# Kernel optimization log

Measured on AMD Instinct MI355X. Metric: run time of the kernel, lower is better.

Reference implementation:

```python
import jax, jax.numpy as jnp
import numpy as np

B = 32
NODES = [200000, 1024, 256, 32]
CH = [1, 32, 64, 128]
EDGES = [2048000, 262144, 8192]
NCLS = 10


def _wn(V, g):
    # PyTorch weight_norm (dim=0): each output row rescaled to norm g[o]
    return g[:, None] * V / jnp.linalg.norm(V, axis=1, keepdims=True)


def _fgl(x, src, dst, n_out, W, b):
    # x: (B, C_in, N_in); sparse random-adjacency downsample then channel mix
    xt = jnp.moveaxis(x, 2, 0)                                   # (N_in, B, C_in)
    gathered = xt[src]                                           # (E, B, C_in)
    pooled = jax.ops.segment_sum(gathered, dst, num_segments=n_out)  # (N_out, B, C_in)
    return jnp.einsum('nbc,oc->bon', pooled, W) + b[None, :, None]   # (B, C_out, N_out)


def setup_inputs() -> dict:
    key = jax.random.key(0)
    ks = jax.random.split(key, 20)
    d = {}
    d['x'] = jax.random.normal(ks[0], (B, NODES[0]), jnp.float32)
    for i in range(3):
        e = EDGES[i]
        n_in, n_out = NODES[i], NODES[i + 1]
        d[f'edge_src{i}'] = jax.random.randint(ks[1 + 2 * i], (e,), 0, n_in, jnp.int32)
        d[f'edge_dst{i}'] = jnp.sort(jax.random.randint(ks[2 + 2 * i], (e,), 0, n_out, jnp.int32))
    for i in range(3):
        cin, cout = CH[i], CH[i + 1]
        d[f'V{i}'] = jax.random.normal(ks[7 + 3 * i], (cout, cin), jnp.float32) * 0.1
        d[f'g{i}'] = jnp.ones((cout,), jnp.float32)
        d[f'b{i}'] = jnp.zeros((cout,), jnp.float32)
    d['Vfc'] = jax.random.normal(ks[16], (NCLS, CH[-1] * NODES[-1]), jnp.float32) * 0.02
    d['gfc'] = jnp.ones((NCLS,), jnp.float32)
    d['bfc'] = jnp.zeros((NCLS,), jnp.float32)
    return d


def reference(x, edge_src0, edge_dst0, edge_src1, edge_dst1, edge_src2, edge_dst2,
              V0, g0, b0, V1, g1, b1, V2, g2, b2, Vfc, gfc, bfc):
    z = x[:, None, :]                                            # (B, 1, N_in)
    z = _fgl(z, edge_src0, edge_dst0, NODES[1], _wn(V0, g0), b0)  # (B, 32, 1024)
    z = _fgl(z, edge_src1, edge_dst1, NODES[2], _wn(V1, g1), b1)  # (B, 64, 256)
    z = _fgl(z, edge_src2, edge_dst2, NODES[3], _wn(V2, g2), b2)  # (B, 128, 32)
    flat = z.reshape(z.shape[0], -1)                             # (B, 4096)
    return flat @ _wn(Vfc, gfc).T + bfc                          # (B, NCLS)
```

## Files before the change

kernel.cpp:

```cpp
#include <hip/hip_runtime.h>
#include <math.h>

#define N0 200000
#define N1 1024
#define N2 256
#define N3 32
#define NE0 2048000
#define NE1 262144
#define NE2 8192
#define BATCH 32
#define NCLS 10
#define NB 4
#define SRC_PER_B 50000

typedef _Float16 h2 __attribute__((ext_vector_type(2)));
typedef _Float16 h8 __attribute__((ext_vector_type(8)));

__device__ __forceinline__ int lower_bound_i(const int* __restrict__ a, int n, int key) {
    int lo = 0, hi = n;
    while (lo < hi) {
        int mid = (lo + hi) >> 1;
        if (a[mid] < key) lo = mid + 1; else hi = mid;
    }
    return lo;
}

__global__ __launch_bounds__(256) void k_transpose(const float* __restrict__ x,
                                                   h2* __restrict__ xt) {
    __shared__ float tile[32][65];
    const int col0 = blockIdx.x * 64;
    const int tid = threadIdx.x;
    const int c = tid & 63, r0 = tid >> 6;
    #pragma unroll
    for (int r = r0; r < 32; r += 4) {
        int col = col0 + c;
        tile[r][c] = (col < N0) ? x[r * N0 + col] : 0.f;
    }
    __syncthreads();
    const int bb = (tid & 15) * 2, c0 = tid >> 4;
    #pragma unroll
    for (int cc = c0; cc < 64; cc += 16) {
        int col = col0 + cc;
        if (col < N0) {
            h2 v;
            v[0] = (_Float16)tile[bb][cc];
            v[1] = (_Float16)tile[bb + 1][cc];
            xt[col * 16 + (bb >> 1)] = v;
        }
    }
}

__global__ __launch_bounds__(256) void k_bounds(const int* __restrict__ dst,
                                                int* __restrict__ off) {
    int e = blockIdx.x * 256 + threadIdx.x;
    if (e >= NE0) return;
    int d = dst[e];
    int dp = (e == 0) ? -1 : dst[e - 1];
    for (int n = dp + 1; n <= d; ++n) off[n] = e;
    if (e == NE0 - 1) {
        for (int n = d + 1; n <= N1; ++n) off[n] = NE0;
    }
}

__global__ __launch_bounds__(256) void k_partition(const int* __restrict__ src,
                                                   const int* __restrict__ off,
                                                   int* __restrict__ esrc,
                                                   int* __restrict__ bstart) {
    const int n = blockIdx.x;
    const int e0 = off[n];
    const int e1 = off[n + 1];
    const int len = e1 - e0;
    const int tid = threadIdx.x;
    const int wave = tid >> 6, lane = tid & 63;
    const int q0 = e0 + (len * wave) / 4;
    const int q1 = e0 + (len * (wave + 1)) / 4;
    __shared__ int wcnt[4][NB];
    __shared__ int wbase[4][NB];

    int c0 = 0, c1 = 0, c2 = 0, c3 = 0;
    for (int base = q0; base < q1; base += 64) {
        int e = base + lane;
        int b = -1;
        if (e < q1) b = src[e] / SRC_PER_B;
        c0 += __popcll(__ballot(b == 0));
        c1 += __popcll(__ballot(b == 1));
        c2 += __popcll(__ballot(b == 2));
        c3 += __popcll(__ballot(b == 3));
    }
    if (lane == 0) { wcnt[wave][0] = c0; wcnt[wave][1] = c1; wcnt[wave][2] = c2; wcnt[wave][3] = c3; }
    __syncthreads();
    if (tid == 0) {
        int acc = e0;
        #pragma unroll
        for (int b = 0; b < NB; ++b) {
            bstart[n * (NB + 1) + b] = acc;
            #pragma unroll
            for (int w = 0; w < 4; ++w) { wbase[w][b] = acc; acc += wcnt[w][b]; }
        }
        bstart[n * (NB + 1) + NB] = acc;
    }
    __syncthreads();

    int u0 = wbase[wave][0], u1 = wbase[wave][1], u2 = wbase[wave][2], u3 = wbase[wave][3];
    for (int base = q0; base < q1; base += 64) {
        int e = base + lane;
        int s = 0, b = -1;
        if (e < q1) { s = src[e]; b = s / SRC_PER_B; }
        unsigned long long m0 = __ballot(b == 0);
        unsigned long long m1 = __ballot(b == 1);
        unsigned long long m2 = __ballot(b == 2);
        unsigned long long m3 = __ballot(b == 3);
        unsigned long long lt = (1ull << lane) - 1ull;
        if (b == 0)      esrc[u0 + __popcll(m0 & lt)] = s;
        else if (b == 1) esrc[u1 + __popcll(m1 & lt)] = s;
        else if (b == 2) esrc[u2 + __popcll(m2 & lt)] = s;
        else if (b == 3) esrc[u3 + __popcll(m3 & lt)] = s;
        u0 += __popcll(m0); u1 += __popcll(m1); u2 += __popcll(m2); u3 += __popcll(m3);
    }
}

__global__ __launch_bounds__(64) void k_gather0s(const h8* __restrict__ table,
                                                 const int* __restrict__ esrc,
                                                 const int* __restrict__ bstart,
                                                 float* __restrict__ part) {
    const int b = blockIdx.x & (NB - 1);
    const int n = blockIdx.x >> 2;
    const int q0 = bstart[n * (NB + 1) + b];
    const int q1 = bstart[n * (NB + 1) + b + 1];
    const int lane = threadIdx.x;
    const int b4 = lane & 3;
    const int g  = lane >> 2;
    float acc[8] = {0.f, 0.f, 0.f, 0.f, 0.f, 0.f, 0.f, 0.f};
    int e = q0 + g;
    for (; e + 48 < q1; e += 64) {
        int s0 = __builtin_nontemporal_load(esrc + e);
        int s1 = __builtin_nontemporal_load(esrc + e + 16);
        int s2 = __builtin_nontemporal_load(esrc + e + 32);
        int s3 = __builtin_nontemporal_load(esrc + e + 48);
        h8 v0 = table[s0 * 4 + b4];
        h8 v1 = table[s1 * 4 + b4];
        h8 v2 = table[s2 * 4 + b4];
        h8 v3 = table[s3 * 4 + b4];
        #pragma unroll
        for (int i = 0; i < 8; ++i)
            acc[i] += (float)v0[i] + (float)v1[i] + (float)v2[i] + (float)v3[i];
    }
    for (; e < q1; e += 16) {
        int s = __builtin_nontemporal_load(esrc + e);
        h8 v = table[s * 4 + b4];
        #pragma unroll
        for (int i = 0; i < 8; ++i) acc[i] += (float)v[i];
    }
    #pragma unroll
    for (int off = 4; off <= 32; off <<= 1) {
        #pragma unroll
        for (int i = 0; i < 8; ++i) acc[i] += __shfl_xor(acc[i], off);
    }
    if (g == 0) {
        float4 lo = make_float4(acc[0], acc[1], acc[2], acc[3]);
        float4 hi = make_float4(acc[4], acc[5], acc[6], acc[7]);
        float4* p4 = reinterpret_cast<float4*>(part + (size_t)(b * N1 + n) * 32 + b4 * 8);
        p4[0] = lo; p4[1] = hi;
    }
}

__global__ __launch_bounds__(256) void k_reduceP(const float* __restrict__ part,
                                                 _Float16* __restrict__ out) {
    int i = blockIdx.x * 256 + threadIdx.x;
    float s = part[i] + part[N1 * 32 + i] + part[2 * N1 * 32 + i] + part[3 * N1 * 32 + i];
    out[i] = (_Float16)s;
}

__global__ __launch_bounds__(256) void k_gather(const h8* __restrict__ table,
                                                const int* __restrict__ src,
                                                const int* __restrict__ dst,
                                                int nedges,
                                                _Float16* __restrict__ out_h,
                                                float* __restrict__ out_f,
                                                const float* __restrict__ cnt_in,
                                                float* __restrict__ cnt_out,
                                                float* __restrict__ t_out) {
    const int n = blockIdx.x;
    const int e0 = lower_bound_i(dst, nedges, n);
    const int e1 = lower_bound_i(dst, nedges, n + 1);
    const int tid = threadIdx.x;
    const int b4 = tid & 3;
    const int g  = tid >> 2;
    float acc[8] = {0.f, 0.f, 0.f, 0.f, 0.f, 0.f, 0.f, 0.f};
    float tacc = 0.f;
    int e = e0 + g;
    for (; e + 192 < e1; e += 256) {
        int s0 = __builtin_nontemporal_load(src + e);
        int s1 = __builtin_nontemporal_load(src + e + 64);
        int s2 = __builtin_nontemporal_load(src + e + 128);
        int s3 = __builtin_nontemporal_load(src + e + 192);
        h8 v0 = table[s0 * 4 + b4];
        h8 v1 = table[s1 * 4 + b4];
        h8 v2 = table[s2 * 4 + b4];
        h8 v3 = table[s3 * 4 + b4];
        #pragma unroll
        for (int i = 0; i < 8; ++i)
            acc[i] += (float)v0[i] + (float)v1[i] + (float)v2[i] + (float)v3[i];
        if (cnt_in != nullptr && b4 == 0)
            tacc += cnt_in[s0] + cnt_in[s1] + cnt_in[s2] + cnt_in[s3];
    }
    for (; e < e1; e += 64) {
        int s = __builtin_nontemporal_load(src + e);
        h8 v = table[s * 4 + b4];
        #pragma unroll
        for (int i = 0; i < 8; ++i) acc[i] += (float)v[i];
        if (cnt_in != nullptr && b4 == 0) tacc += cnt_in[s];
    }
    __shared__ float red[64][33];
    __shared__ float tred[64];
    #pragma unroll
    for (int i = 0; i < 8; ++i) red[g][b4 * 8 + i] = acc[i];
    if (b4 == 0) tred[g] = tacc;
    __syncthreads();
    #pragma unroll
    for (int s = 32; s >= 1; s >>= 1) {
        if (g < s) {
            #pragma unroll
            for (int i = 0; i < 8; ++i)
                red[g][b4 * 8 + i] += red[g + s][b4 * 8 + i];
            if (b4 == 0) tred[g] += tred[g + s];
        }
        __syncthreads();
    }
    if (tid < 32) {
        float v = red[0][tid];
        if (out_h != nullptr) out_h[n * 32 + tid] = (_Float16)v;
        if (out_f != nullptr) out_f[n * 32 + tid] = v;
    } else if (tid == 32 && cnt_out != nullptr) {
        cnt_out[n] = (float)(e1 - e0);
    } else if (tid == 33 && t_out != nullptr) {
        t_out[n] = tred[0];
    }
}

__global__ __launch_bounds__(256) void k_out(
    const float* __restrict__ V0, const float* __restrict__ g0, const float* __restrict__ b0,
    const float* __restrict__ V1, const float* __restrict__ g1, const float* __restrict__ b1,
    const float* __restrict__ V2, const float* __restrict__ g2, const float* __restrict__ b2,
    const float* __restrict__ Vfc, const float* __restrict__ gfc, const float* __restrict__ bfc,
    const float* __restrict__ S2, const float* __restrict__ T2, const float* __restrict__ cnt2,
    float* __restrict__ out) {
    const int k = blockIdx.x;
    const int tid = threadIdx.x;
    __shared__ float w0[32], u[64], v[64], p[128], q[128], r[128];
    __shared__ float redA[8][32], redB[8][32], redC[8][32], redD[8][32];
    __shared__ float nnred[4];
    __shared__ float M[32];
    __shared__ float scale_s, Kc_s;

    if (tid < 32) {
        float val = V0[tid];
        w0[tid] = g0[tid] * val / fabsf(val);
    }
    __syncthreads();
    if (tid < 64) {
        float nn = 0.f;
        #pragma unroll
        for (int c = 0; c < 32; ++c) { float t = V1[tid * 32 + c]; nn += t * t; }
        float inv = g1[tid] * rsqrtf(nn);
        float su = 0.f, sv = 0.f;
        #pragma unroll
        for (int c = 0; c < 32; ++c) {
            float w = V1[tid * 32 + c] * inv;
            su += w * w0[c]; sv += w * b0[c];
        }
        u[tid] = su; v[tid] = sv;
    }
    __syncthreads();
    if (tid < 128) {
        float nn = 0.f;
        #pragma unroll
        for (int c = 0; c < 64; ++c) { float t = V2[tid * 64 + c]; nn += t * t; }
        float inv = g2[tid] * rsqrtf(nn);
        float sp = 0.f, sq = 0.f, sr = 0.f;
        #pragma unroll
        for (int c = 0; c < 64; ++c) {
            float w = V2[tid * 64 + c] * inv;
            sp += w * u[c]; sq += w * v[c]; sr += w * b1[c];
        }
        p[tid] = sp; q[tid] = sq; r[tid] = sr;
    }
    __syncthreads();

    const int n3 = tid & 31, og = tid >> 5;
    float nn = 0.f, mk = 0.f, mq = 0.f, mr = 0.f, mb = 0.f;
    #pragma unroll
    for (int i = 0; i < 16; ++i) {
        int o = og + 8 * i;
        float w = Vfc[k * 4096 + tid + 256 * i];
        nn += w * w;
        mk += w * p[o]; mq += w * q[o]; mr += w * r[o]; mb += w * b2[o];
    }
    #pragma unroll
    for (int off = 32; off; off >>= 1) nn += __shfl_xor(nn, off);
    if ((tid & 63) == 0) nnred[tid >> 6] = nn;
    redA[og][n3] = mk; redB[og][n3] = mq; redC[og][n3] = mr; redD[og][n3] = mb;
    __syncthreads();
    if (tid == 0) {
        float s = nnred[0] + nnred[1] + nnred[2] + nnred[3];
        scale_s = gfc[k] * rsqrtf(s);
    }
    __syncthreads();
    if (tid < 32) {
        float smk = 0.f, smq = 0.f, smr = 0.f, smb = 0.f;
        #pragma unroll
        for (int i = 0; i < 8; ++i) {
            smk += redA[i][tid]; smq += redB[i][tid];
            smr += redC[i][tid]; smb += redD[i][tid];
        }
        float scale = scale_s;
        M[tid] = scale * smk;
        float kcp = scale * (smq * T2[tid] + smr * cnt2[tid] + smb);
        #pragma unroll
        for (int off = 16; off; off >>= 1) kcp += __shfl_xor(kcp, off);
        if (tid == 0) Kc_s = kcp + bfc[k];
    }
    __syncthreads();
    if (tid < 32) {
        int b = tid;
        float s = 0.f;
        #pragma unroll
        for (int n = 0; n < 32; ++n) s += M[n] * S2[n * 32 + b];
        out[b * NCLS + k] = s + Kc_s;
    }
}

extern "C" void kernel_launch(void* const* d_in, const int* in_sizes, int n_in,
                              void* d_out, int out_size, void* d_ws, size_t ws_size,
                              hipStream_t stream) {
    const float* x   = (const float*)d_in[0];
    const int* src0  = (const int*)d_in[1];
    const int* dst0  = (const int*)d_in[2];
    const int* src1  = (const int*)d_in[3];
    const int* dst1  = (const int*)d_in[4];
    const int* src2  = (const int*)d_in[5];
    const int* dst2  = (const int*)d_in[6];
    const float* V0  = (const float*)d_in[7];
    const float* g0  = (const float*)d_in[8];
    const float* b0  = (const float*)d_in[9];
    const float* V1  = (const float*)d_in[10];
    const float* g1  = (const float*)d_in[11];
    const float* b1  = (const float*)d_in[12];
    const float* V2  = (const float*)d_in[13];
    const float* g2  = (const float*)d_in[14];
    const float* b2  = (const float*)d_in[15];
    const float* Vfc = (const float*)d_in[16];
    const float* gfc = (const float*)d_in[17];
    const float* bfc = (const float*)d_in[18];

    char* ws = (char*)d_ws;
    _Float16* xt  = (_Float16*)(ws);
    int* esrc     = (int*)(ws + 12800000);
    int* off      = (int*)(ws + 20992000);
    int* bstart   = (int*)(ws + 20996352);
    float* P0p    = (float*)(ws + 21016832);
    _Float16* P0h = (_Float16*)(ws + 21541120);
    _Float16* S1h = (_Float16*)(ws + 21606656);
    float* cnt1   = (float*)(ws + 21623040);
    float* S2     = (float*)(ws + 21624064);
    float* T2     = (float*)(ws + 21628160);
    float* cnt2   = (float*)(ws + 21628288);

    k_transpose<<<(N0 + 63) / 64, 256, 0, stream>>>(x, (h2*)xt);
    k_bounds<<<NE0 / 256, 256, 0, stream>>>(dst0, off);
    k_partition<<<N1, 256, 0, stream>>>(src0, off, esrc, bstart);
    k_gather0s<<<N1 * NB, 64, 0, stream>>>((const h8*)xt, esrc, bstart, P0p);
    k_reduceP<<<(N1 * 32) / 256, 256, 0, stream>>>(P0p, P0h);
    k_gather<<<N2, 256, 0, stream>>>((const h8*)P0h, src1, dst1, NE1,
                                     S1h, nullptr, nullptr, cnt1, nullptr);
    k_gather<<<N3, 256, 0, stream>>>((const h8*)S1h, src2, dst2, NE2,
                                     nullptr, S2, cnt1, cnt2, T2);
    k_out<<<NCLS, 256, 0, stream>>>(V0, g0, b0, V1, g1, b1, V2, g2, b2,
                                    Vfc, gfc, bfc, S2, T2, cnt2, (float*)d_out);
}
```

Before: 77.78 us.

## Fuse small tail kernels, drop bounds pass, last-block reduction in gather0

Removes the k_bounds pass by having k_partition binary-search dst0 directly, and folds k_reduceP into k_gather0s through an atomic last-block-done counter. The layer-2 gather and the output projection are merged into one 1024-thread k_tail kernel. k_gather0s also moves to 128-thread blocks with a shared-memory reduction. The aim is to cut kernel launch count and tiny-grid launch overhead, at the cost of serialising the final reduction on one block and running the tail on a single CU.

```diff
diff --git a/kernel.cpp b/kernel.cpp
--- a/kernel.cpp
+++ b/kernel.cpp
@@ -12,6 +12,7 @@
 #define NCLS 10
 #define NB 4
 #define SRC_PER_B 50000
+#define G0_BLOCKS (N1 * NB)
 
 typedef _Float16 h2 __attribute__((ext_vector_type(2)));
 typedef _Float16 h8 __attribute__((ext_vector_type(8)));
@@ -50,27 +51,17 @@
     }
 }
 
-__global__ __launch_bounds__(256) void k_bounds(const int* __restrict__ dst,
-                                                int* __restrict__ off) {
-    int e = blockIdx.x * 256 + threadIdx.x;
-    if (e >= NE0) return;
-    int d = dst[e];
-    int dp = (e == 0) ? -1 : dst[e - 1];
-    for (int n = dp + 1; n <= d; ++n) off[n] = e;
-    if (e == NE0 - 1) {
-        for (int n = d + 1; n <= N1; ++n) off[n] = NE0;
-    }
-}
-
 __global__ __launch_bounds__(256) void k_partition(const int* __restrict__ src,
-                                                   const int* __restrict__ off,
+                                                   const int* __restrict__ dst,
                                                    int* __restrict__ esrc,
-                                                   int* __restrict__ bstart) {
+                                                   int* __restrict__ bstart,
+                                                   int* __restrict__ gcnt) {
     const int n = blockIdx.x;
-    const int e0 = off[n];
-    const int e1 = off[n + 1];
+    const int tid = threadIdx.x;
+    if (n == 0 && tid == 0) *gcnt = 0;
+    const int e0 = lower_bound_i(dst, NE0, n);
+    const int e1 = lower_bound_i(dst, NE0, n + 1);
     const int len = e1 - e0;
-    const int tid = threadIdx.x;
     const int wave = tid >> 6, lane = tid & 63;
     const int q0 = e0 + (len * wave) / 4;
     const int q1 = e0 + (len * (wave + 1)) / 4;
@@ -119,24 +110,26 @@
     }
 }
 
-__global__ __launch_bounds__(64) void k_gather0s(const h8* __restrict__ table,
-                                                 const int* __restrict__ esrc,
-                                                 const int* __restrict__ bstart,
-                                                 float* __restrict__ part) {
+__global__ __launch_bounds__(128) void k_gather0s(const h8* __restrict__ table,
+                                                  const int* __restrict__ esrc,
+                                                  const int* __restrict__ bstart,
+                                                  float* __restrict__ part,
+                                                  _Float16* __restrict__ p0h,
+                                                  int* __restrict__ gcnt) {
     const int b = blockIdx.x & (NB - 1);
     const int n = blockIdx.x >> 2;
     const int q0 = bstart[n * (NB + 1) + b];
     const int q1 = bstart[n * (NB + 1) + b + 1];
-    const int lane = threadIdx.x;
-    const int b4 = lane & 3;
-    const int g  = lane >> 2;
+    const int tid = threadIdx.x;
+    const int b4 = tid & 3;
+    const int g  = tid >> 2;
     float acc[8] = {0.f, 0.f, 0.f, 0.f, 0.f, 0.f, 0.f, 0.f};
     int e = q0 + g;
-    for (; e + 48 < q1; e += 64) {
+    for (; e + 96 < q1; e += 128) {
         int s0 = __builtin_nontemporal_load(esrc + e);
-        int s1 = __builtin_nontemporal_load(esrc + e + 16);
-        int s2 = __builtin_nontemporal_load(esrc + e + 32);
-        int s3 = __builtin_nontemporal_load(esrc + e + 48);
+        int s1 = __builtin_nontemporal_load(esrc + e + 32);
+        int s2 = __builtin_nontemporal_load(esrc + e + 64);
+        int s3 = __builtin_nontemporal_load(esrc + e + 96);
         h8 v0 = table[s0 * 4 + b4];
         h8 v1 = table[s1 * 4 + b4];
         h8 v2 = table[s2 * 4 + b4];
@@ -145,55 +138,71 @@
         for (int i = 0; i < 8; ++i)
             acc[i] += (float)v0[i] + (float)v1[i] + (float)v2[i] + (float)v3[i];
     }
-    for (; e < q1; e += 16) {
+    for (; e < q1; e += 32) {
         int s = __builtin_nontemporal_load(esrc + e);
         h8 v = table[s * 4 + b4];
         #pragma unroll
         for (int i = 0; i < 8; ++i) acc[i] += (float)v[i];
     }
-    #pragma unroll
-    for (int off = 4; off <= 32; off <<= 1) {
-        #pragma unroll
-        for (int i = 0; i < 8; ++i) acc[i] += __shfl_xor(acc[i], off);
-    }
-    if (g == 0) {
-        float4 lo = make_float4(acc[0], acc[1], acc[2], acc[3]);
-        float4 hi = make_float4(acc[4], acc[5], acc[6], acc[7]);
-        float4* p4 = reinterpret_cast<float4*>(part + (size_t)(b * N1 + n) * 32 + b4 * 8);
-        p4[0] = lo; p4[1] = hi;
-    }
-}
-
-__global__ __launch_bounds__(256) void k_reduceP(const float* __restrict__ part,
-                                                 _Float16* __restrict__ out) {
-    int i = blockIdx.x * 256 + threadIdx.x;
-    float s = part[i] + part[N1 * 32 + i] + part[2 * N1 * 32 + i] + part[3 * N1 * 32 + i];
-    out[i] = (_Float16)s;
-}
-
-__global__ __launch_bounds__(256) void k_gather(const h8* __restrict__ table,
-                                                const int* __restrict__ src,
-                                                const int* __restrict__ dst,
-                                                int nedges,
-                                                _Float16* __restrict__ out_h,
-                                                float* __restrict__ out_f,
-                                                const float* __restrict__ cnt_in,
-                                                float* __restrict__ cnt_out,
-                                                float* __restrict__ t_out) {
+    __shared__ float red[32][33];
+    #pragma unroll
+    for (int i = 0; i < 8; ++i) red[g][b4 * 8 + i] = acc[i];
+    __syncthreads();
+    #pragma unroll
+    for (int s = 16; s >= 1; s >>= 1) {
+        if (g < s) {
+            #pragma unroll
+            for (int i = 0; i < 8; ++i)
+                red[g][b4 * 8 + i] += red[g + s][b4 * 8 + i];
+        }
+        __syncthreads();
+    }
+    if (tid < 32) part[(b * N1 + n) * 32 + tid] = red[0][tid];
+
+    __shared__ int isLast;
+    __threadfence();
+    __syncthreads();
+    if (tid == 0) {
+        int old = atomicAdd(gcnt, 1);
+        isLast = (old == G0_BLOCKS - 1) ? 1 : 0;
+    }
+    __syncthreads();
+    if (isLast) {
+        __threadfence();
+        const float4* p4 = (const float4*)part;
+        h2* out2 = (h2*)p0h;
+        for (int i = tid; i < 8192; i += 128) {
+            float4 a = p4[i], c = p4[8192 + i], d = p4[16384 + i], f = p4[24576 + i];
+            float sx = a.x + c.x + d.x + f.x;
+            float sy = a.y + c.y + d.y + f.y;
+            float sz = a.z + c.z + d.z + f.z;
+            float sw = a.w + c.w + d.w + f.w;
+            h2 lo; lo[0] = (_Float16)sx; lo[1] = (_Float16)sy;
+            h2 hi; hi[0] = (_Float16)sz; hi[1] = (_Float16)sw;
+            out2[i * 2] = lo; out2[i * 2 + 1] = hi;
+        }
+        if (tid == 0) *gcnt = 0;
+    }
+}
+
+__global__ __launch_bounds__(256) void k_gather1(const h8* __restrict__ table,
+                                                 const int* __restrict__ src,
+                                                 const int* __restrict__ dst,
+                                                 _Float16* __restrict__ out_h,
+                                                 float* __restrict__ cnt_out) {
     const int n = blockIdx.x;
-    const int e0 = lower_bound_i(dst, nedges, n);
-    const int e1 = lower_bound_i(dst, nedges, n + 1);
+    const int e0 = lower_bound_i(dst, NE1, n);
+    const int e1 = lower_bound_i(dst, NE1, n + 1);
     const int tid = threadIdx.x;
     const int b4 = tid & 3;
     const int g  = tid >> 2;
     float acc[8] = {0.f, 0.f, 0.f, 0.f, 0.f, 0.f, 0.f, 0.f};
-    float tacc = 0.f;
     int e = e0 + g;
     for (; e + 192 < e1; e += 256) {
-        int s0 = __builtin_nontemporal_load(src + e);
-        int s1 = __builtin_nontemporal_load(src + e + 64);
-        int s2 = __builtin_nontemporal_load(src + e + 128);
-        int s3 = __builtin_nontemporal_load(src + e + 192);
+        int s0 = src[e];
+        int s1 = src[e + 64];
+        int s2 = src[e + 128];
+        int s3 = src[e + 192];
         h8 v0 = table[s0 * 4 + b4];
         h8 v1 = table[s1 * 4 + b4];
         h8 v2 = table[s2 * 4 + b4];
@@ -201,21 +210,16 @@
         #pragma unroll
         for (int i = 0; i < 8; ++i)
             acc[i] += (float)v0[i] + (float)v1[i] + (float)v2[i] + (float)v3[i];
-        if (cnt_in != nullptr && b4 == 0)
-            tacc += cnt_in[s0] + cnt_in[s1] + cnt_in[s2] + cnt_in[s3];
     }
     for (; e < e1; e += 64) {
-        int s = __builtin_nontemporal_load(src + e);
+        int s = src[e];
         h8 v = table[s * 4 + b4];
         #pragma unroll
         for (int i = 0; i < 8; ++i) acc[i] += (float)v[i];
-        if (cnt_in != nullptr && b4 == 0) tacc += cnt_in[s];
     }
     __shared__ float red[64][33];
-    __shared__ float tred[64];
     #pragma unroll
     for (int i = 0; i < 8; ++i) red[g][b4 * 8 + i] = acc[i];
-    if (b4 == 0) tred[g] = tacc;
     __syncthreads();
     #pragma unroll
     for (int s = 32; s >= 1; s >>= 1) {
@@ -223,40 +227,65 @@
             #pragma unroll
             for (int i = 0; i < 8; ++i)
                 red[g][b4 * 8 + i] += red[g + s][b4 * 8 + i];
-            if (b4 == 0) tred[g] += tred[g + s];
         }
         __syncthreads();
     }
-    if (tid < 32) {
-        float v = red[0][tid];
-        if (out_h != nullptr) out_h[n * 32 + tid] = (_Float16)v;
-        if (out_f != nullptr) out_f[n * 32 + tid] = v;
-    } else if (tid == 32 && cnt_out != nullptr) {
-        cnt_out[n] = (float)(e1 - e0);
-    } else if (tid == 33 && t_out != nullptr) {
-        t_out[n] = tred[0];
-    }
-}
-
-__global__ __launch_bounds__(256) void k_out(
+    if (tid < 32) out_h[n * 32 + tid] = (_Float16)red[0][tid];
+    else if (tid == 32) cnt_out[n] = (float)(e1 - e0);
+}
+
+__global__ __launch_bounds__(1024) void k_tail(
+    const h8* __restrict__ tableS1, const int* __restrict__ src2,
+    const int* __restrict__ dst2, const float* __restrict__ cnt1,
     const float* __restrict__ V0, const float* __restrict__ g0, const float* __restrict__ b0,
     const float* __restrict__ V1, const float* __restrict__ g1, const float* __restrict__ b1,
     const float* __restrict__ V2, const float* __restrict__ g2, const float* __restrict__ b2,
     const float* __restrict__ Vfc, const float* __restrict__ gfc, const float* __restrict__ bfc,
-    const float* __restrict__ S2, const float* __restrict__ T2, const float* __restrict__ cnt2,
     float* __restrict__ out) {
-    const int k = blockIdx.x;
-    const int tid = threadIdx.x;
-    __shared__ float w0[32], u[64], v[64], p[128], q[128], r[128];
-    __shared__ float redA[8][32], redB[8][32], redC[8][32], redD[8][32];
-    __shared__ float nnred[4];
-    __shared__ float M[32];
-    __shared__ float scale_s, Kc_s;
+    const int tid = threadIdx.x;
+    __shared__ float S2_l[32][33];
+    __shared__ float T2_l[32], cnt2_l[32];
+    __shared__ float w0[32], u[64], v[64], p[128], q[128], r[128], b2_l[128];
+    __shared__ float M_l[10][33], Kc_l[10];
+
+    {
+        const int n = tid >> 5;
+        const int l32 = tid & 31;
+        const int b4 = l32 & 3;
+        const int g  = l32 >> 2;
+        const int e0 = lower_bound_i(dst2, NE2, n);
+        const int e1 = lower_bound_i(dst2, NE2, n + 1);
+        float acc[8] = {0.f, 0.f, 0.f, 0.f, 0.f, 0.f, 0.f, 0.f};
+        float tacc = 0.f;
+        for (int e = e0 + g; e < e1; e += 8) {
+            int s = src2[e];
+            h8 vv = tableS1[s * 4 + b4];
+            #pragma unroll
+            for (int i = 0; i < 8; ++i) acc[i] += (float)vv[i];
+            if (b4 == 0) tacc += cnt1[s];
+        }
+        #pragma unroll
+        for (int off = 4; off <= 16; off <<= 1) {
+            #pragma unroll
+            for (int i = 0; i < 8; ++i) acc[i] += __shfl_xor(acc[i], off);
+            tacc += __shfl_xor(tacc, off);
+        }
+        if (g == 0) {
+            #pragma unroll
+            for (int i = 0; i < 8; ++i) S2_l[n][b4 * 8 + i] = acc[i];
+            if (b4 == 0) { T2_l[n] = tacc; cnt2_l[n] = (float)(e1 - e0); }
+        }
+    }
+    __syncthreads();
 
     if (tid < 32) {
         float val = V0[tid];
         w0[tid] = g0[tid] * val / fabsf(val);
     }
+    if (tid >= 896) {
+        int i = tid - 896;
+        b2_l[i] = b2[i];
+    }
     __syncthreads();
     if (tid < 64) {
         float nn = 0.f;
@@ -287,46 +316,36 @@
     }
     __syncthreads();
 
-    const int n3 = tid & 31, og = tid >> 5;
-    float nn = 0.f, mk = 0.f, mq = 0.f, mr = 0.f, mb = 0.f;
-    #pragma unroll
-    for (int i = 0; i < 16; ++i) {
-        int o = og + 8 * i;
-        float w = Vfc[k * 4096 + tid + 256 * i];
-        nn += w * w;
-        mk += w * p[o]; mq += w * q[o]; mr += w * r[o]; mb += w * b2[o];
-    }
-    #pragma unroll
-    for (int off = 32; off; off >>= 1) nn += __shfl_xor(nn, off);
-    if ((tid & 63) == 0) nnred[tid >> 6] = nn;
-    redA[og][n3] = mk; redB[og][n3] = mq; redC[og][n3] = mr; redD[og][n3] = mb;
-    __syncthreads();
-    if (tid == 0) {
-        float s = nnred[0] + nnred[1] + nnred[2] + nnred[3];
-        scale_s = gfc[k] * rsqrtf(s);
-    }
-    __syncthreads();
-    if (tid < 32) {
-        float smk = 0.f, smq = 0.f, smr = 0.f, smb = 0.f;
-        #pragma unroll
-        for (int i = 0; i < 8; ++i) {
-            smk += redA[i][tid]; smq += redB[i][tid];
-            smr += redC[i][tid]; smb += redD[i][tid];
-        }
-        float scale = scale_s;
-        M[tid] = scale * smk;
-        float kcp = scale * (smq * T2[tid] + smr * cnt2[tid] + smb);
-        #pragma unroll
-        for (int off = 16; off; off >>= 1) kcp += __shfl_xor(kcp, off);
-        if (tid == 0) Kc_s = kcp + bfc[k];
-    }
-    __syncthreads();
-    if (tid < 32) {
-        int b = tid;
-        float s = 0.f;
-        #pragma unroll
-        for (int n = 0; n < 32; ++n) s += M[n] * S2[n * 32 + b];
-        out[b * NCLS + k] = s + Kc_s;
+    {
+        const int k = tid >> 5, n3 = tid & 31;
+        if (k < NCLS) {
+            float nn = 0.f, mk = 0.f, mq = 0.f, mr = 0.f, mb = 0.f;
+            #pragma unroll 8
+            for (int o = 0; o < 128; ++o) {
+                float w = Vfc[k * 4096 + o * 32 + n3];
+                nn += w * w;
+                mk += w * p[o]; mq += w * q[o]; mr += w * r[o]; mb += w * b2_l[o];
+            }
+            #pragma unroll
+            for (int off = 16; off; off >>= 1) nn += __shfl_xor(nn, off);
+            float scale = gfc[k] * rsqrtf(nn);
+            M_l[k][n3] = scale * mk;
+            float kcp = scale * (mq * T2_l[n3] + mr * cnt2_l[n3] + mb);
+            #pragma unroll
+            for (int off = 16; off; off >>= 1) kcp += __shfl_xor(kcp, off);
+            if (n3 == 0) Kc_l[k] = kcp + bfc[k];
+        }
+    }
+    __syncthreads();
+
+    {
+        const int k = tid >> 5, b = tid & 31;
+        if (k < NCLS) {
+            float s = 0.f;
+            #pragma unroll
+            for (int n = 0; n < 32; ++n) s += M_l[k][n] * S2_l[n][b];
+            out[b * NCLS + k] = s + Kc_l[k];
+        }
     }
 }
 
@@ -356,25 +375,19 @@
     char* ws = (char*)d_ws;
     _Float16* xt  = (_Float16*)(ws);
     int* esrc     = (int*)(ws + 12800000);
-    int* off      = (int*)(ws + 20992000);
-    int* bstart   = (int*)(ws + 20996352);
-    float* P0p    = (float*)(ws + 21016832);
-    _Float16* P0h = (_Float16*)(ws + 21541120);
-    _Float16* S1h = (_Float16*)(ws + 21606656);
-    float* cnt1   = (float*)(ws + 21623040);
-    float* S2     = (float*)(ws + 21624064);
-    float* T2     = (float*)(ws + 21628160);
-    float* cnt2   = (float*)(ws + 21628288);
+    int* bstart   = (int*)(ws + 20992000);
+    float* P0p    = (float*)(ws + 21012480);
+    _Float16* P0h = (_Float16*)(ws + 21536768);
+    _Float16* S1h = (_Float16*)(ws + 21602304);
+    float* cnt1   = (float*)(ws + 21618688);
+    int* gcnt     = (int*)(ws + 21619712);
 
     k_transpose<<<(N0 + 63) / 64, 256, 0, stream>>>(x, (h2*)xt);
-    k_bounds<<<NE0 / 256, 256, 0, stream>>>(dst0, off);
-    k_partition<<<N1, 256, 0, stream>>>(src0, off, esrc, bstart);
-    k_gather0s<<<N1 * NB, 64, 0, stream>>>((const h8*)xt, esrc, bstart, P0p);
-    k_reduceP<<<(N1 * 32) / 256, 256, 0, stream>>>(P0p, P0h);
-    k_gather<<<N2, 256, 0, stream>>>((const h8*)P0h, src1, dst1, NE1,
-                                     S1h, nullptr, nullptr, cnt1, nullptr);
-    k_gather<<<N3, 256, 0, stream>>>((const h8*)S1h, src2, dst2, NE2,
-                                     nullptr, S2, cnt1, cnt2, T2);
-    k_out<<<NCLS, 256, 0, stream>>>(V0, g0, b0, V1, g1, b1, V2, g2, b2,
-                                    Vfc, gfc, bfc, S2, T2, cnt2, (float*)d_out);
-}
+    k_partition<<<N1, 256, 0, stream>>>(src0, dst0, esrc, bstart, gcnt);
+    k_gather0s<<<G0_BLOCKS, 128, 0, stream>>>((const h8*)xt, esrc, bstart,
+                                              P0p, P0h, gcnt);
+    k_gather1<<<N2, 256, 0, stream>>>((const h8*)P0h, src1, dst1, S1h, cnt1);
+    k_tail<<<1, 1024, 0, stream>>>((const h8*)S1h, src2, dst2, cnt1,
+                                   V0, g0, b0, V1, g1, b1, V2, g2, b2,
+                                   Vfc, gfc, bfc, (float*)d_out);
+}
```

Result: slower. 273.7 us (+251.9%).
